# Optimization experiments

Hardware: AMD Instinct MI355X
Metric: run time of the kernel (lower is better)

## Reference

```python
import jax, jax.numpy as jnp
import numpy as np

N_VISIBLE = 50000
N_HIDDEN = 5000
N_NODES = N_VISIBLE + N_HIDDEN
N_EDGES = 1_000_000
BATCH = 128


def setup_inputs() -> dict:
    key = jax.random.key(0)
    k1, k2, k3, k4, k5 = jax.random.split(key, 5)
    # parameters, initialized as in the torch module
    linear = 0.05 * (2.0 * jax.random.uniform(k1, (N_NODES,), dtype=jnp.float32) - 1.0)
    quadratic = 5.0 * (2.0 * jax.random.uniform(k2, (N_EDGES,), dtype=jnp.float32) - 1.0)
    # bipartite visible-hidden edges -> CSR-like flat buffers (via segment ids)
    flat_adj = jax.random.randint(k3, (N_EDGES,), 0, N_VISIBLE, dtype=jnp.int32).astype(jnp.int64)  # visible endpoint per edge
    seg_ids = jax.random.randint(k4, (N_EDGES,), 0, N_HIDDEN, dtype=jnp.int32).astype(jnp.int64)    # hidden bin per edge
    flat_j_idx = jnp.arange(N_EDGES, dtype=jnp.int64)  # quadratic coefficient index per flat entry
    hidden_idx = jnp.arange(N_HIDDEN, dtype=jnp.int64) + N_VISIBLE
    # observed spin configurations in {0,1} (mapped to +-1 inside reference)
    s = jax.random.randint(k5, (BATCH, N_NODES), 0, 2, dtype=jnp.int32)
    return {
        "linear": linear,
        "quadratic": quadratic,
        "s": s,
        "flat_adj": flat_adj,
        "flat_j_idx": flat_j_idx,
        "seg_ids": seg_ids,
        "hidden_idx": hidden_idx,
        "n_hidden": N_HIDDEN,
    }


def reference(linear, quadratic, s, flat_adj, flat_j_idx, seg_ids, hidden_idx, n_hidden):
    """Per-hidden-unit effective field + conditional spin expectation.

    eff[b, k] = linear[hidden_idx[k]]
                + sum_{e : seg_ids[e]==k} quadratic[flat_j_idx[e]] * s_pm[b, flat_adj[e]]
    returns tanh(-eff)  (conditional expectation of hidden spins given visibles)
    """
    s_pm = (2 * s - 1).astype(linear.dtype)                 # {0,1} -> {-1,+1}, (B, N)
    w = quadratic[flat_j_idx]                               # (E,)
    contrib = s_pm[:, flat_adj].T * w[:, None]              # (E, B) gathered neighbor terms
    field = jax.ops.segment_sum(contrib, seg_ids, num_segments=n_hidden)  # (K, B)
    eff = field.T + linear[hidden_idx][None, :]             # (B, K)
    return jnp.tanh(-eff)
```

## Files before the change

### kernel.cpp

```cpp
#include <hip/hip_runtime.h>
#include <math.h>
#include <stdint.h>

#define NV 50000
#define NH 5000
#define NN 55000
#define NCB 313
#define BCAP 4096
#define KSLOT 384
#define CHUNK 4096


__device__ __forceinline__ uint32_t selmask(uint32_t word, uint32_t bsh) {
#if __has_builtin(__builtin_amdgcn_sbfe)
    return (uint32_t)__builtin_amdgcn_sbfe((int)word, bsh, 1u);
#else
    return (uint32_t)((int32_t)(word << (31u - bsh)) >> 31);
#endif
}

__global__ void __launch_bounds__(256) pack_zero_kernel(
        const int* __restrict__ s, uint32_t* __restrict__ bits,
        uint32_t* __restrict__ coarse_cnt) {
    if (blockIdx.x == 0)
        for (int i = threadIdx.x; i < NCB; i += 256) coarse_cnt[i] = 0u;
    int tid = blockIdx.x * 256 + threadIdx.x;
    int v = tid >> 2;
    int g = tid & 3;
    if (v >= NV) return;
    const int* col = s + (size_t)g * 32 * NN + v;
    uint32_t w = 0;
#pragma unroll
    for (int j = 0; j < 32; ++j)
        w |= (uint32_t)(col[(size_t)j * NN] & 1) << j;
    bits[(size_t)v * 4 + g] = w;
}

__global__ void __launch_bounds__(256) coarse_split_kernel(
        const int4* __restrict__ seg4, const int4* __restrict__ adj4,
        const float4* __restrict__ quad4,
        uint32_t* __restrict__ coarse_cnt, uint2* __restrict__ recs, int E) {
    __shared__ uint32_t hist[320];
    __shared__ uint32_t loc[320];
    __shared__ uint32_t cur[NCB];
    __shared__ uint32_t gbase[NCB];
    __shared__ __align__(16) uint2 st[CHUNK];
    __shared__ uint32_t dst[CHUNK];
    const int tid = threadIdx.x;
    for (int i = tid; i < 320; i += 256) hist[i] = 0u;
    __syncthreads();

    const int c0 = blockIdx.x * CHUNK;
    const int nloc = min(CHUNK, E - c0);
    int kreg[16];
#pragma unroll
    for (int j = 0; j < 4; ++j) {
        int t4 = (c0 >> 2) + j * 256 + tid;
        bool ok = t4 < ((c0 + nloc) >> 2);
        int4 sg = ok ? seg4[t4] : make_int4(-1, -1, -1, -1);
        kreg[j * 4 + 0] = sg.x; kreg[j * 4 + 1] = sg.y;
        kreg[j * 4 + 2] = sg.z; kreg[j * 4 + 3] = sg.w;
        if (ok) {
            atomicAdd(&hist[sg.x >> 4], 1u);
            atomicAdd(&hist[sg.y >> 4], 1u);
            atomicAdd(&hist[sg.z >> 4], 1u);
            atomicAdd(&hist[sg.w >> 4], 1u);
        }
    }
    __syncthreads();
    for (int i = tid; i < NCB; i += 256)
        gbase[i] = atomicAdd(&coarse_cnt[i], hist[i]);
    for (int i = tid; i < 320; i += 256) loc[i] = hist[i];
    __syncthreads();
    for (int d = 1; d < 320; d <<= 1) {
        uint32_t v0 = 0, v1 = 0;
        int i1 = tid + 256;
        if (tid >= d) v0 = loc[tid - d];
        if (i1 < 320 && i1 >= d) v1 = loc[i1 - d];
        __syncthreads();
        if (tid >= d) loc[tid] += v0;
        if (i1 < 320 && i1 >= d) loc[i1] += v1;
        __syncthreads();
    }
    for (int i = tid; i < NCB; i += 256) cur[i] = loc[i] - hist[i];
    __syncthreads();
#pragma unroll
    for (int j = 0; j < 4; ++j) {
        int t4 = (c0 >> 2) + j * 256 + tid;
        if (t4 < ((c0 + nloc) >> 2)) {
            int4 a = adj4[t4];
            float4 q = quad4[t4];
#pragma unroll
            for (int cmp = 0; cmp < 4; ++cmp) {
                int k = kreg[j * 4 + cmp];
                int v = (cmp == 0) ? a.x : (cmp == 1) ? a.y : (cmp == 2) ? a.z : a.w;
                float w = (cmp == 0) ? q.x : (cmp == 1) ? q.y : (cmp == 2) ? q.z : q.w;
                int bk = k >> 4;
                uint32_t slot = atomicAdd(&cur[bk], 1u);
                uint32_t rank = gbase[bk] + (slot - (loc[bk] - hist[bk]));
                st[slot] = make_uint2((uint32_t)v | ((uint32_t)(k & 15) << 16),
                                      __float_as_uint(w));
                dst[slot] = (rank < BCAP) ? (uint32_t)bk * BCAP + rank : ~0u;
            }
        }
    }
    __syncthreads();
    for (int i = tid; i < nloc; i += 256) {
        uint32_t d = dst[i];
        if (d != ~0u) recs[d] = st[i];
    }
}

__global__ void __launch_bounds__(256) quarter_field_kernel(
        const uint32_t* __restrict__ coarse_cnt, const uint2* __restrict__ recs,
        const uint4* __restrict__ bits4, const float* __restrict__ linear,
        float* __restrict__ out) {
    const int x = blockIdx.x;
    const int j = (x & 7) * 157 + (x >> 3);
    const int bkt = j >> 2;
    const int q = j & 3;
    if (bkt >= NCB) return;
    const int tid = threadIdx.x;

    __shared__ uint32_t cur4[4];
    __shared__ float swp[4];
    __shared__ __align__(16) uint2 st4[4][KSLOT];
    __shared__ __align__(16) uint32_t rows[2][5][KSLOT];
    __shared__ float part[2][256];

    if (tid < 4) cur4[tid] = 0u;
    __syncthreads();

    int cnt = (int)min(coarse_cnt[bkt], (uint32_t)BCAP);
    const uint2* region = recs + (size_t)bkt * BCAP;
    for (int i = tid; i < cnt; i += 256) {
        uint2 r = region[i];
        int kl = (int)((r.x >> 16) & 15u);
        if ((kl >> 2) == q) {
            uint32_t p = atomicAdd(&cur4[kl & 3], 1u);
            if (p < KSLOT) st4[kl & 3][p] = r;
        }
    }
    __syncthreads();

    const int b = tid & 127;
    const int grp = tid >> 7;
    const uint32_t bsh = (uint32_t)(b & 31);
    const int widx = b >> 5;

    for (int rnd = 0; rnd < 2; ++rnd) {
        int kl = rnd * 2 + grp;
        int c = min((int)cur4[kl], KSLOT);
        int T8 = (c + 7) & ~7;
        float sw = 0.f;
        for (int t = c + b; t < T8; t += 128) rows[grp][4][t] = 0u;
        for (int t = b; t < c; t += 128) {
            uint2 r = st4[kl][t];
            uint4 mw = bits4[r.x & 0xFFFFu];
            rows[grp][0][t] = mw.x;
            rows[grp][1][t] = mw.y;
            rows[grp][2][t] = mw.z;
            rows[grp][3][t] = mw.w;
            rows[grp][4][t] = r.y;
            sw += __uint_as_float(r.y);
        }
#pragma unroll
        for (int off = 32; off; off >>= 1) sw += __shfl_down(sw, off);
        if ((tid & 63) == 0) swp[tid >> 6] = sw;
        __syncthreads();

#pragma unroll
        for (int kk = 0; kk < 2; ++kk) {
            int T8k = (min((int)cur4[rnd * 2 + kk], KSLOT) + 7) & ~7;
            const uint32_t* mrow = rows[kk][widx];
            const uint32_t* wrow = rows[kk][4];
            float a0 = 0.f, a1 = 0.f, a2 = 0.f, a3 = 0.f;
            for (int i = grp * 4; i < T8k; i += 8) {
                uint4 mm = *(const uint4*)(mrow + i);
                uint4 ww = *(const uint4*)(wrow + i);
                a0 += __uint_as_float(ww.x & selmask(mm.x, bsh));
                a1 += __uint_as_float(ww.y & selmask(mm.y, bsh));
                a2 += __uint_as_float(ww.z & selmask(mm.z, bsh));
                a3 += __uint_as_float(ww.w & selmask(mm.w, bsh));
            }
            part[kk][tid] = (a0 + a1) + (a2 + a3);
        }
        __syncthreads();
        if (tid < 128) {
            int k0 = bkt * 16 + q * 4 + rnd * 2;
            if (k0 + 1 < NH) {
                float acc0 = part[0][tid] + part[0][tid + 128];
                float acc1 = part[1][tid] + part[1][tid + 128];
                float e0 = 2.f * acc0 - (swp[0] + swp[1]) + linear[NV + k0];
                float e1 = 2.f * acc1 - (swp[2] + swp[3]) + linear[NV + k0 + 1];
                float2 o = make_float2(tanhf(-e0), tanhf(-e1));
                *(float2*)(out + (size_t)tid * NH + k0) = o;
            }
        }
        __syncthreads();
    }
}

extern "C" void kernel_launch(void* const* d_in, const int* in_sizes, int n_in,
                              void* d_out, int out_size, void* d_ws, size_t ws_size,
                              hipStream_t stream) {
    const float* linear = (const float*)d_in[0];
    const float* quad   = (const float*)d_in[1];
    const int*   s      = (const int*)d_in[2];
    const int*   adj    = (const int*)d_in[3];
    const int*   seg    = (const int*)d_in[5];
    const int E = in_sizes[5];
    float* out = (float*)d_out;

    char* ws = (char*)d_ws;
    uint32_t* bits       = (uint32_t*)(ws);
    uint32_t* coarse_cnt = (uint32_t*)(ws + 800000);
    uint2*    recs       = (uint2*)   (ws + 801280);

    pack_zero_kernel<<<(NV * 4 + 255) / 256, 256, 0, stream>>>(s, bits, coarse_cnt);
    const int nchunk = (E + CHUNK - 1) / CHUNK;
    coarse_split_kernel<<<nchunk, 256, 0, stream>>>(
        (const int4*)seg, (const int4*)adj, (const float4*)quad, coarse_cnt, recs, E);
    quarter_field_kernel<<<1256, 256, 0, stream>>>(coarse_cnt, recs, (const uint4*)bits,
                                                   linear, out);
}
```

Before: 133.7 us.

## Fuse record scatter with bitmask gather and process four hidden units per pass

The quarter_field kernel now gathers the packed spin bitmasks directly while scanning the bucket records. This removes the intermediate st4 staging buffer and the two-round structure. The row buffers are widened to hold all four hidden units at once, the weight sums are accumulated during the scan with shared atomics, and results are written as float4. The shared-memory footprint grows, which could lower occupancy. The selmask helper also drops the sbfe builtin in favour of a shift-based form.

```diff
diff --git a/kernel.cpp b/kernel.cpp
--- a/kernel.cpp
+++ b/kernel.cpp
@@ -12,11 +12,7 @@
 
 
 __device__ __forceinline__ uint32_t selmask(uint32_t word, uint32_t bsh) {
-#if __has_builtin(__builtin_amdgcn_sbfe)
-    return (uint32_t)__builtin_amdgcn_sbfe((int)word, bsh, 1u);
-#else
     return (uint32_t)((int32_t)(word << (31u - bsh)) >> 31);
-#endif
 }
 
 __global__ void __launch_bounds__(256) pack_zero_kernel(
@@ -124,22 +120,64 @@
 
     __shared__ uint32_t cur4[4];
     __shared__ float swp[4];
-    __shared__ __align__(16) uint2 st4[4][KSLOT];
-    __shared__ __align__(16) uint32_t rows[2][5][KSLOT];
-    __shared__ float part[2][256];
+    __shared__ __align__(16) uint32_t rows[4][5][KSLOT];
+    __shared__ float part[4][256];
 
     if (tid < 4) cur4[tid] = 0u;
+    else if (tid < 8) swp[tid - 4] = 0.f;
     __syncthreads();
 
     int cnt = (int)min(coarse_cnt[bkt], (uint32_t)BCAP);
-    const uint2* region = recs + (size_t)bkt * BCAP;
-    for (int i = tid; i < cnt; i += 256) {
-        uint2 r = region[i];
-        int kl = (int)((r.x >> 16) & 15u);
-        if ((kl >> 2) == q) {
-            uint32_t p = atomicAdd(&cur4[kl & 3], 1u);
-            if (p < KSLOT) st4[kl & 3][p] = r;
-        }
+    const uint4* region4 = (const uint4*)(recs + (size_t)bkt * BCAP);
+    float sw0 = 0.f, sw1 = 0.f, sw2 = 0.f, sw3 = 0.f;
+    for (int i2 = tid; i2 * 2 < cnt; i2 += 256) {
+        uint4 rr = region4[i2];
+#pragma unroll
+        for (int h = 0; h < 2; ++h) {
+            int idx = i2 * 2 + h;
+            if (idx >= cnt) break;
+            uint32_t rx = h ? rr.z : rr.x;
+            uint32_t ry = h ? rr.w : rr.y;
+            int kl = (int)((rx >> 16) & 15u);
+            if ((kl >> 2) == q) {
+                int l = kl & 3;
+                uint32_t p = atomicAdd(&cur4[l], 1u);
+                if (p < KSLOT) {
+                    uint4 mw = bits4[rx & 0xFFFFu];
+                    rows[l][0][p] = mw.x;
+                    rows[l][1][p] = mw.y;
+                    rows[l][2][p] = mw.z;
+                    rows[l][3][p] = mw.w;
+                    rows[l][4][p] = ry;
+                    float wv = __uint_as_float(ry);
+                    if (l == 0) sw0 += wv;
+                    else if (l == 1) sw1 += wv;
+                    else if (l == 2) sw2 += wv;
+                    else sw3 += wv;
+                }
+            }
+        }
+    }
+#pragma unroll
+    for (int off = 32; off; off >>= 1) {
+        sw0 += __shfl_down(sw0, off);
+        sw1 += __shfl_down(sw1, off);
+        sw2 += __shfl_down(sw2, off);
+        sw3 += __shfl_down(sw3, off);
+    }
+    if ((tid & 63) == 0) {
+        atomicAdd(&swp[0], sw0);
+        atomicAdd(&swp[1], sw1);
+        atomicAdd(&swp[2], sw2);
+        atomicAdd(&swp[3], sw3);
+    }
+    __syncthreads();
+
+    if (tid < 4) {
+        int c = min((int)cur4[tid], KSLOT);
+        int T8 = (c + 7) & ~7;
+        for (int t = c; t < T8; ++t) rows[tid][4][t] = 0u;
+        cur4[tid] = (uint32_t)T8;
     }
     __syncthreads();
 
@@ -147,57 +185,37 @@
     const int grp = tid >> 7;
     const uint32_t bsh = (uint32_t)(b & 31);
     const int widx = b >> 5;
-
-    for (int rnd = 0; rnd < 2; ++rnd) {
-        int kl = rnd * 2 + grp;
-        int c = min((int)cur4[kl], KSLOT);
-        int T8 = (c + 7) & ~7;
-        float sw = 0.f;
-        for (int t = c + b; t < T8; t += 128) rows[grp][4][t] = 0u;
-        for (int t = b; t < c; t += 128) {
-            uint2 r = st4[kl][t];
-            uint4 mw = bits4[r.x & 0xFFFFu];
-            rows[grp][0][t] = mw.x;
-            rows[grp][1][t] = mw.y;
-            rows[grp][2][t] = mw.z;
-            rows[grp][3][t] = mw.w;
-            rows[grp][4][t] = r.y;
-            sw += __uint_as_float(r.y);
-        }
-#pragma unroll
-        for (int off = 32; off; off >>= 1) sw += __shfl_down(sw, off);
-        if ((tid & 63) == 0) swp[tid >> 6] = sw;
-        __syncthreads();
-
-#pragma unroll
-        for (int kk = 0; kk < 2; ++kk) {
-            int T8k = (min((int)cur4[rnd * 2 + kk], KSLOT) + 7) & ~7;
-            const uint32_t* mrow = rows[kk][widx];
-            const uint32_t* wrow = rows[kk][4];
-            float a0 = 0.f, a1 = 0.f, a2 = 0.f, a3 = 0.f;
-            for (int i = grp * 4; i < T8k; i += 8) {
-                uint4 mm = *(const uint4*)(mrow + i);
-                uint4 ww = *(const uint4*)(wrow + i);
-                a0 += __uint_as_float(ww.x & selmask(mm.x, bsh));
-                a1 += __uint_as_float(ww.y & selmask(mm.y, bsh));
-                a2 += __uint_as_float(ww.z & selmask(mm.z, bsh));
-                a3 += __uint_as_float(ww.w & selmask(mm.w, bsh));
+#pragma unroll
+    for (int kk = 0; kk < 4; ++kk) {
+        int T8 = (int)cur4[kk];
+        const uint32_t* mrow = rows[kk][widx];
+        const uint32_t* wrow = rows[kk][4];
+        float a0 = 0.f, a1 = 0.f, a2 = 0.f, a3 = 0.f;
+        for (int i = grp * 4; i < T8; i += 8) {
+            uint4 mm = *(const uint4*)(mrow + i);
+            uint4 ww = *(const uint4*)(wrow + i);
+            a0 += __uint_as_float(ww.x & selmask(mm.x, bsh));
+            a1 += __uint_as_float(ww.y & selmask(mm.y, bsh));
+            a2 += __uint_as_float(ww.z & selmask(mm.z, bsh));
+            a3 += __uint_as_float(ww.w & selmask(mm.w, bsh));
+        }
+        part[kk][tid] = (a0 + a1) + (a2 + a3);
+    }
+    __syncthreads();
+
+    if (tid < 128) {
+        int k0 = bkt * 16 + q * 4;
+        if (k0 + 3 < NH) {
+            float4 o;
+            float* op = (float*)&o;
+#pragma unroll
+            for (int kk = 0; kk < 4; ++kk) {
+                float acc = part[kk][tid] + part[kk][tid + 128];
+                float e = 2.f * acc - swp[kk] + linear[NV + k0 + kk];
+                op[kk] = tanhf(-e);
             }
-            part[kk][tid] = (a0 + a1) + (a2 + a3);
-        }
-        __syncthreads();
-        if (tid < 128) {
-            int k0 = bkt * 16 + q * 4 + rnd * 2;
-            if (k0 + 1 < NH) {
-                float acc0 = part[0][tid] + part[0][tid + 128];
-                float acc1 = part[1][tid] + part[1][tid + 128];
-                float e0 = 2.f * acc0 - (swp[0] + swp[1]) + linear[NV + k0];
-                float e1 = 2.f * acc1 - (swp[2] + swp[3]) + linear[NV + k0 + 1];
-                float2 o = make_float2(tanhf(-e0), tanhf(-e1));
-                *(float2*)(out + (size_t)tid * NH + k0) = o;
-            }
-        }
-        __syncthreads();
+            *(float4*)(out + (size_t)tid * NH + k0) = o;
+        }
     }
 }
 
```

Measured after the change: 142.1 us. 1.06x slower.
